# Kernel optimization log

Hardware: AMD Instinct MI355X
Metric: run time of the kernel (lower is better)

Reference implementation:

```python
import jax, jax.numpy as jnp
import numpy as np
import math

B, S, D, H = 2, 2048, 1024, 16
HD = D // H


def _rms_norm(x, scale):
    # norm over (seq, d_model) jointly per batch element, as in the source
    b, s, d = x.shape
    ff_rms = jnp.sqrt(jnp.sum(x * x, axis=(1, 2))) * (s * d) ** -0.5  # (B,)
    return scale[None, :s, :] * (x / ff_rms[:, None, None])


def _rope(x):
    # faithful to _generate_rope_matrix: theta = 10000^(-2*(i-1)/D) (note i-1)
    b, s, d = x.shape
    i = jnp.arange(d // 2, dtype=jnp.float32)
    theta = 10000.0 ** (-2.0 * (i - 1.0) / d)            # (D/2,)
    ang = jnp.arange(s, dtype=jnp.float32)[:, None] * theta[None, :]  # (S, D/2)
    cos, sin = jnp.cos(ang), jnp.sin(ang)
    xp = x.reshape(b, s, d // 2, 2)
    xe, xo = xp[..., 0], xp[..., 1]
    # out = x @ R[pos]; R block [[cos,-sin],[sin,cos]] per pair
    oe = xe * cos + xo * sin
    oo = -xe * sin + xo * cos
    return jnp.stack([oe, oo], axis=-1).reshape(b, s, d)


def _alibi_mask(s, h):
    r = jnp.arange(s)
    dist = r[:, None] - r[None, :]                        # row j - col i
    base = jnp.where(dist < 0, -jnp.inf, -dist.astype(jnp.float32))  # (S,S)
    ratio = 2.0 ** (-8.0 / h)
    slopes = ratio ** jnp.arange(1, h + 1, dtype=jnp.float32)        # (H,)
    return base[None, :, :] * slopes[:, None, None]       # (H,S,S)


def setup_inputs() -> dict:
    key = jax.random.key(0)
    ks = jax.random.split(key, 9)
    p = lambda k, shp: jax.random.normal(k, shp, jnp.float32) * 0.02
    return {
        "x": jax.random.normal(ks[0], (B, S, D), jnp.float32),
        "Wq": p(ks[1], (D, D)), "Wk": p(ks[2], (D, D)),
        "Wv": p(ks[3], (D, D)), "Wo": p(ks[4], (D, D)),
        "scale1": jnp.ones((S, D), jnp.float32),
        "scale2": jnp.ones((S, D), jnp.float32),
        "W1": p(ks[5], (D, D)), "b1": jnp.zeros((D,), jnp.float32),
        "Wg": p(ks[6], (D, D)), "bg": jnp.zeros((D,), jnp.float32),
        "Wl": p(ks[7], (D, D)), "bl": jnp.zeros((D,), jnp.float32),
        "beta": jnp.ones((1,), jnp.float32),
    }


def reference(x, Wq, Wk, Wv, Wo, scale1, scale2, W1, b1, Wg, bg, Wl, bl, beta):
    b, s, d = x.shape
    # --- attention sublayer ---
    h = _rms_norm(x, scale1)
    q = _rope(h @ Wq)
    k = _rope(h @ Wk)
    v = _rope(h @ Wv)
    qh = q.reshape(b, s, H, HD).transpose(0, 2, 1, 3)  # (B,H,S,HD)
    kh = k.reshape(b, s, H, HD).transpose(0, 2, 1, 3)
    vh = v.reshape(b, s, H, HD).transpose(0, 2, 1, 3)
    mask = _alibi_mask(s, H)                           # (H,S,S)
    scores = jnp.einsum("bhqd,bhkd->bhqk", qh, kh) * (1.0 / math.sqrt(HD))
    probs = jax.nn.softmax(scores + mask[None], axis=-1)
    o = jnp.einsum("bhqk,bhkd->bhqd", probs, vh)
    o = o.transpose(0, 2, 1, 3).reshape(b, s, d)
    x_res_1 = x + o @ Wo
    # --- FFN sublayer: Linear -> SwiGLU ---
    h2 = _rms_norm(x_res_1, scale2) @ W1 + b1
    g = h2 @ Wg + bg
    swish_gate = g * jax.nn.sigmoid(beta * g)
    ffn = swish_gate * (h2 @ Wl + bl)
    return x_res_1 + ffn
```

## Files before the change

### kernel.cpp

```cpp
#include <hip/hip_runtime.h>
#include <hip/hip_bf16.h>

typedef __attribute__((ext_vector_type(8))) short bf16x8;
typedef __attribute__((ext_vector_type(4))) float f32x4;
typedef __attribute__((ext_vector_type(4))) int int4v;

#define DEV static __device__ __forceinline__

DEV float b2f(unsigned short u) { union { unsigned int i; float f; } c; c.i = ((unsigned int)u) << 16; return c.f; }
DEV unsigned short f2b(float f) {
  __hip_bfloat16 h = __float2bfloat16(f);
  unsigned short u; __builtin_memcpy(&u, &h, 2); return u;
}

DEV void gload16(const void* g, void* l) {
  __builtin_amdgcn_global_load_lds(
      (const __attribute__((address_space(1))) unsigned int*)(g),
      (__attribute__((address_space(3))) unsigned int*)(l), 16, 0, 0);
}

__global__ __launch_bounds__(256) void k_transpose_w7(const float* __restrict__ Wq,
                                                      const float* __restrict__ Wk,
                                                      const float* __restrict__ Wv,
                                                      const float* __restrict__ Wo,
                                                      const float* __restrict__ W1,
                                                      const float* __restrict__ Wg,
                                                      const float* __restrict__ Wl,
                                                      unsigned short* __restrict__ WT) {
  __shared__ float tile[32][33];
  const float* W;
  switch (blockIdx.z) {
    case 0: W = Wq; break; case 1: W = Wk; break; case 2: W = Wv; break;
    case 3: W = Wo; break; case 4: W = W1; break; case 5: W = Wg; break;
    default: W = Wl; break;
  }
  unsigned short* dst = WT + (size_t)blockIdx.z * 1048576;
  const int tx = threadIdx.x & 31, ty = threadIdx.x >> 5;
  const int c0 = blockIdx.x * 32, r0 = blockIdx.y * 32;
#pragma unroll
  for (int i = 0; i < 4; ++i)
    tile[ty + i * 8][tx] = W[(size_t)(r0 + ty + i * 8) * 1024 + c0 + tx];
  __syncthreads();
#pragma unroll
  for (int i = 0; i < 4; ++i)
    dst[(size_t)(c0 + ty + i * 8) * 1024 + r0 + tx] = f2b(tile[tx][ty + i * 8]);
}

__global__ __launch_bounds__(256) void k_reduce_sq(const float* __restrict__ x,
                                                   float* __restrict__ sums) {
  const int b = blockIdx.y;
  const float4* xb = (const float4*)(x + (size_t)b * 2097152);
  float s = 0.f;
  for (int i = blockIdx.x * 256 + threadIdx.x; i < 524288; i += 256 * gridDim.x) {
    float4 v = xb[i];
    s += v.x * v.x + v.y * v.y + v.z * v.z + v.w * v.w;
  }
  __shared__ float red[256];
  red[threadIdx.x] = s;
  __syncthreads();
  for (int st = 128; st > 0; st >>= 1) {
    if (threadIdx.x < st) red[threadIdx.x] += red[threadIdx.x + st];
    __syncthreads();
  }
  if (threadIdx.x == 0) atomicAdd(&sums[b], red[0]);
}

__global__ __launch_bounds__(256) void k_rmsnorm(const float* __restrict__ x,
                                                 const float* __restrict__ scale,
                                                 const float* __restrict__ sums,
                                                 unsigned short* __restrict__ out) {
  const int idx = blockIdx.x * 256 + threadIdx.x;
  const int e = idx * 4;
  const int m = e >> 10, d = e & 1023;
  const int b = m >> 11, s = m & 2047;
  const float inv = rsqrtf(sums[b] * (1.0f / 2097152.0f));
  float4 xv = *(const float4*)(x + (size_t)e);
  float4 sv = *(const float4*)(scale + (size_t)s * 1024 + d);
  ushort4 o;
  o.x = f2b(xv.x * sv.x * inv); o.y = f2b(xv.y * sv.y * inv);
  o.z = f2b(xv.z * sv.z * inv); o.w = f2b(xv.w * sv.w * inv);
  *(ushort4*)(out + e) = o;
}

template <int EPI, int NREP>
__global__ __launch_bounds__(256) void k_gemm(const unsigned short* __restrict__ A,
                                              const unsigned short* __restrict__ Bt,
                                              void* __restrict__ Cout,
                                              const float* __restrict__ aux,
                                              const float* __restrict__ aux2,
                                              const float* __restrict__ x1p,
                                              const float* __restrict__ betap,
                                              const int N,
                                              float* __restrict__ ss) {
  constexpr int BN = NREP * 32;
  __shared__ short As[2][128 * 64];
  __shared__ short Bs[2][BN * 64];
  const int tid = threadIdx.x;
  const int w = tid >> 6, l = tid & 63;
  const int brow = blockIdx.y * 128;
  const int bcol = blockIdx.x * (EPI == 4 ? 64 : BN);
  const int wr = (w >> 1) * 64;
  const int wc = (EPI == 4) ? (w & 1) * 32 : (w & 1) * (NREP * 16);
  const int lr = l >> 3, lg = l & 7;
  f32x4 acc[4][NREP] = {};
  const short* Ag = (const short*)A;
  const short* Bg = (const short*)Bt;

  auto STAGE = [&](int buf, int k0) {
#pragma unroll
    for (int p = 0; p < 4; ++p) {
      const int row = p * 32 + w * 8 + lr;
      gload16(Ag + (size_t)(brow + row) * 1024 + k0 + lg * 8,
              (char*)&As[buf][0] + (size_t)(p * 32 + w * 8) * 128);
    }
#pragma unroll
    for (int p = 0; p < NREP; ++p) {
      const int row = p * 32 + w * 8 + lr;
      size_t goff;
      if (EPI == 4 && p >= 2)
        goff = (size_t)1048576 + (size_t)(bcol + row - 64) * 1024;
      else
        goff = (size_t)(bcol + row) * 1024;
      gload16(Bg + goff + k0 + lg * 8,
              (char*)&Bs[buf][0] + (size_t)(p * 32 + w * 8) * 128);
    }
  };

  STAGE(0, 0);
  __syncthreads();
  int cur = 0;
  for (int t = 0; t < 16; ++t) {
    if (t < 15) STAGE(cur ^ 1, (t + 1) * 64);
#pragma unroll
    for (int kk = 0; kk < 2; ++kk) {
      const int g0 = kk * 4 + (l >> 4);
      bf16x8 af[4], bfr[NREP];
#pragma unroll
      for (int m = 0; m < 4; ++m)
        af[m] = *(const bf16x8*)(&As[cur][0] + (wr + m * 16 + (l & 15)) * 64 + g0 * 8);
#pragma unroll
      for (int n = 0; n < NREP; ++n) {
        int bsrow;
        if (EPI == 4) bsrow = (n < 2) ? (wc + n * 16 + (l & 15)) : (64 + wc + (n - 2) * 16 + (l & 15));
        else bsrow = wc + n * 16 + (l & 15);
        bfr[n] = *(const bf16x8*)(&Bs[cur][0] + bsrow * 64 + g0 * 8);
      }
      __builtin_amdgcn_s_setprio(1);
#pragma unroll
      for (int m = 0; m < 4; ++m)
#pragma unroll
        for (int n = 0; n < NREP; ++n)
          acc[m][n] = __builtin_amdgcn_mfma_f32_16x16x32_bf16(af[m], bfr[n], acc[m][n], 0, 0, 0);
      __builtin_amdgcn_s_setprio(0);
    }
    __syncthreads();
    cur ^= 1;
  }
  const int rr = (l >> 4) * 4, cc = l & 15;
  if (EPI == 5) {
    const bool dorope = (bcol < 2048);
    if (dorope) {
      float th[NREP];
#pragma unroll
      for (int n = 0; n < NREP; ++n)
        th[n] = exp2f(-((float)(((bcol + wc + n * 16 + cc) & 1023) >> 1) - 1.0f) * 0.0259525627f);
#pragma unroll
      for (int m = 0; m < 4; ++m)
#pragma unroll
        for (int n = 0; n < NREP; ++n) {
          const int col = bcol + wc + n * 16 + cc;
#pragma unroll
          for (int j = 0; j < 4; ++j) {
            const int row = brow + wr + m * 16 + rr + j;
            const float vo = acc[m][n][j];
            const float vp = __shfl_xor(vo, 1);
            float sn, cs;
            __sincosf((float)(row & 2047) * th[n], &sn, &cs);
            const float r = (cc & 1) ? (cs * vo - sn * vp) : (cs * vo + sn * vp);
            ((unsigned short*)Cout)[(size_t)row * N + col] = f2b(r);
          }
        }
    } else {
#pragma unroll
      for (int m = 0; m < 4; ++m)
#pragma unroll
        for (int n = 0; n < NREP; ++n) {
          const int col = bcol + wc + n * 16 + cc;
#pragma unroll
          for (int j = 0; j < 4; ++j) {
            const int row = brow + wr + m * 16 + rr + j;
            ((unsigned short*)Cout)[(size_t)row * N + col] = f2b(acc[m][n][j]);
          }
        }
    }
    return;
  }
  if (EPI == 4) {
    const float bt = betap[0];
#pragma unroll
    for (int m = 0; m < 4; ++m)
#pragma unroll
      for (int nn = 0; nn < 2; ++nn) {
        const int col = bcol + wc + nn * 16 + cc;
#pragma unroll
        for (int j = 0; j < 4; ++j) {
          const int row = brow + wr + m * 16 + rr + j;
          const float gv = acc[m][nn][j] + aux[col];
          const float lv = acc[m][nn + 2][j] + aux2[col];
          const float sw = gv / (1.f + __expf(-bt * gv));
          ((float*)Cout)[(size_t)row * 1024 + col] = x1p[(size_t)row * 1024 + col] + sw * lv;
        }
      }
    return;
  }
  float sq = 0.f;
#pragma unroll
  for (int m = 0; m < 4; ++m)
#pragma unroll
    for (int n = 0; n < NREP; ++n) {
      const int col = bcol + wc + n * 16 + cc;
#pragma unroll
      for (int j = 0; j < 4; ++j) {
        const int row = brow + wr + m * 16 + rr + j;
        float v = acc[m][n][j];
        if (EPI == 1) {
          const float v2 = aux[(size_t)row * N + col] + v;
          ((float*)Cout)[(size_t)row * N + col] = v2;
          sq += v2 * v2;
        } else {
          ((unsigned short*)Cout)[(size_t)row * N + col] = f2b(v + aux[col]);
        }
      }
    }
  if (EPI == 1) {
#pragma unroll
    for (int off = 1; off < 64; off <<= 1) sq += __shfl_xor(sq, off);
    if (l == 0) atomicAdd(&ss[brow >> 11], sq);
  }
}

__global__ __launch_bounds__(256) void k_transpose_v(const unsigned short* __restrict__ qkv,
                                                     unsigned short* __restrict__ vt) {
  __shared__ unsigned short tile[32][33];
  const int tx = threadIdx.x & 31, ty = threadIdx.x >> 5;
  const int bh = blockIdx.z;
  const int b = bh >> 4, h = bh & 15;
  const int d0 = blockIdx.x * 32, s0 = blockIdx.y * 32;
#pragma unroll
  for (int i = 0; i < 4; ++i)
    tile[ty + i * 8][tx] = qkv[(size_t)(b * 2048 + s0 + ty + i * 8) * 3072 + 2048 + h * 64 + d0 + tx];
  __syncthreads();
  const float sv = (float)(s0 + tx);
  const int par = ty & 1;
#pragma unroll
  for (int i = 0; i < 4; ++i) {
    const int dsec = h * 64 + d0 + ty + i * 8;
    const float th = exp2f(-((float)(dsec >> 1) - 1.0f) * 0.0259525627f);
    float sn, cs;
    __sincosf(sv * th, &sn, &cs);
    const float vo = b2f(tile[tx][ty + i * 8]);
    const float vp = b2f(tile[tx][(ty ^ 1) + i * 8]);
    const float r = par ? (cs * vo - sn * vp) : (cs * vo + sn * vp);
    vt[((size_t)bh * 64 + d0 + ty + i * 8) * 2048 + s0 + tx] = f2b(r);
  }
}

__global__ __launch_bounds__(256) void k_attn(const unsigned short* __restrict__ qkv,
                                              const unsigned short* __restrict__ vt,
                                              unsigned short* __restrict__ o) {
  __shared__ short Ks[2][4096];
  __shared__ short Vs[2][4096];
  __shared__ short Ps[8][1280];
  const int id = blockIdx.x;
  const int xcd = id & 7, q = id >> 3;
  const int p = q & 15, g = (q >> 4) * 8 + xcd;
  const int h = g & 15, b = g >> 4;
  const int qtA = p, qtB = 31 - p;
  const int nA = qtA + 1, nB = qtB + 1;
  const int tid = threadIdx.x, w = tid >> 6, l = tid & 63;
  const int cc = l & 15, hi = l >> 4;
  const int qwA = qtA * 64 + w * 16, qwB = qtB * 64 + w * 16;
  const short* qg = (const short*)qkv;
  bf16x8 aqA0, aqA1, aqB0, aqB1;
  {
    const short* baseA = qg + (size_t)(b * 2048 + qwA + cc) * 3072 + h * 64 + hi * 8;
    aqA0 = *(const bf16x8*)baseA;
    aqA1 = *(const bf16x8*)(baseA + 32);
    const short* baseB = qg + (size_t)(b * 2048 + qwB + cc) * 3072 + h * 64 + hi * 8;
    aqB0 = *(const bf16x8*)baseB;
    aqB1 = *(const bf16x8*)(baseB + 32);
  }
  const float slope2 = exp2f(-0.5f * (float)(h + 1)) * 1.44269504f;
  const float C1 = 0.125f * 1.44269504f;
  const float step = slope2 * 64.f;
  bf16x8 onesf;
#pragma unroll
  for (int z = 0; z < 8; ++z) onesf[z] = (short)0x3F80;
  f32x4 oaccA[4] = {}, oaccB[4] = {};
  f32x4 rsA = {}, rsB = {};
  float baseA4[4], baseB4[4];
#pragma unroll
  for (int n = 0; n < 4; ++n) {
    baseA4[n] = slope2 * (float)(n * 16 + cc - qwA - hi * 4);
    baseB4[n] = slope2 * (float)(n * 16 + cc - qwB - hi * 4);
  }
  short* PwA = &Ps[w][0];
  short* PwB = &Ps[w + 4][0];
  const int c0 = tid, c1 = tid + 256;
  const int r0 = c0 >> 3, g0c = c0 & 7;
  const int r1 = c1 >> 3, g1c = c1 & 7;
  const int s0 = r0 * 64 + ((g0c ^ (r0 & 7)) * 8);
  const int s1 = r1 * 64 + ((g1c ^ (r1 & 7)) * 8);
  const short* kbase = qg + (size_t)(b * 2048) * 3072 + 1024 + h * 64;
  const short* vbase = (const short*)vt + (size_t)(b * 16 + h) * 64 * 2048;
  *(int4v*)(&Ks[0][s0]) = *(const int4v*)(kbase + (size_t)r0 * 3072 + g0c * 8);
  *(int4v*)(&Ks[0][s1]) = *(const int4v*)(kbase + (size_t)r1 * 3072 + g1c * 8);
  *(int4v*)(&Vs[0][s0]) = *(const int4v*)(vbase + (size_t)r0 * 2048 + g0c * 8);
  *(int4v*)(&Vs[0][s1]) = *(const int4v*)(vbase + (size_t)r1 * 2048 + g1c * 8);
  __syncthreads();

  auto sm_pv = [&](f32x4 (&sacc)[4], f32x4 (&oacc)[4], f32x4& rs, float (&base)[4],
                   short* Pw, const int qw, const bool domask, const int kv0,
                   const short* Vsc) {
#pragma unroll
    for (int n = 0; n < 4; ++n) {
#pragma unroll
      for (int j = 0; j < 4; ++j) {
        float v = fmaf(sacc[n][j], C1, base[n] - slope2 * (float)j);
        if (domask) {
          const int kvg = kv0 + n * 16 + cc;
          const int qrow = qw + hi * 4 + j;
          if (kvg > qrow) v = -1e30f;
        }
        Pw[(hi * 4 + j) * 80 + n * 16 + cc] = (short)f2b(exp2f(v));
      }
      base[n] += step;
    }
    __builtin_amdgcn_s_setprio(1);
#pragma unroll
    for (int kk2 = 0; kk2 < 2; ++kk2) {
      bf16x8 pf = *(const bf16x8*)(Pw + cc * 80 + kk2 * 32 + hi * 8);
      rs = __builtin_amdgcn_mfma_f32_16x16x32_bf16(pf, onesf, rs, 0, 0, 0);
#pragma unroll
      for (int n = 0; n < 4; ++n) {
        const int dr = n * 16 + cc;
        bf16x8 vf = *(const bf16x8*)(Vsc + dr * 64 + (((kk2 * 4 + hi) ^ (dr & 7)) * 8));
        oacc[n] = __builtin_amdgcn_mfma_f32_16x16x32_bf16(pf, vf, oacc[n], 0, 0, 0);
      }
    }
    __builtin_amdgcn_s_setprio(0);
  };

  int cur = 0;
  for (int t = 0; t < nB; ++t) {
    int4v kr0, kr1, vr0, vr1;
    const bool havenext = (t + 1 < nB);
    if (havenext) {
      const size_t k0n = (size_t)(t + 1) * 64;
      kr0 = *(const int4v*)(kbase + (k0n + r0) * 3072 + g0c * 8);
      kr1 = *(const int4v*)(kbase + (k0n + r1) * 3072 + g1c * 8);
      vr0 = *(const int4v*)(vbase + (size_t)r0 * 2048 + k0n + g0c * 8);
      vr1 = *(const int4v*)(vbase + (size_t)r1 * 2048 + k0n + g1c * 8);
    }
    const int kv0 = t * 64;
    const short* Ksc = &Ks[cur][0];
    const short* Vsc = &Vs[cur][0];
    const bool doA = (t < nA);
    f32x4 sB[4] = {}, sA[4] = {};
    __builtin_amdgcn_s_setprio(1);
#pragma unroll
    for (int kk = 0; kk < 2; ++kk) {
      const int g0r = kk * 4 + hi;
      const bf16x8 aqk = kk ? aqB1 : aqB0;
#pragma unroll
      for (int n = 0; n < 4; ++n) {
        const int col = n * 16 + cc;
        bf16x8 bk = *(const bf16x8*)(Ksc + col * 64 + ((g0r ^ (col & 7)) * 8));
        sB[n] = __builtin_amdgcn_mfma_f32_16x16x32_bf16(aqk, bk, sB[n], 0, 0, 0);
      }
    }
    if (doA) {
#pragma unroll
      for (int kk = 0; kk < 2; ++kk) {
        const int g0r = kk * 4 + hi;
        const bf16x8 aqk = kk ? aqA1 : aqA0;
#pragma unroll
        for (int n = 0; n < 4; ++n) {
          const int col = n * 16 + cc;
          bf16x8 bk = *(const bf16x8*)(Ksc + col * 64 + ((g0r ^ (col & 7)) * 8));
          sA[n] = __builtin_amdgcn_mfma_f32_16x16x32_bf16(aqk, bk, sA[n], 0, 0, 0);
        }
      }
    }
    __builtin_amdgcn_s_setprio(0);
    sm_pv(sB, oaccB, rsB, baseB4, PwB, qwB, t == nB - 1, kv0, Vsc);
    if (doA) sm_pv(sA, oaccA, rsA, baseA4, PwA, qwA, t == nA - 1, kv0, Vsc);
    if (havenext) {
      const int nxt = cur ^ 1;
      *(int4v*)(&Ks[nxt][s0]) = kr0;
      *(int4v*)(&Ks[nxt][s1]) = kr1;
      *(int4v*)(&Vs[nxt][s0]) = vr0;
      *(int4v*)(&Vs[nxt][s1]) = vr1;
    }
    __syncthreads();
    cur ^= 1;
  }
  {
    const int rr = hi * 4;
#pragma unroll
    for (int n = 0; n < 4; ++n)
#pragma unroll
      for (int j = 0; j < 4; ++j) {
        const int row = qwA + rr + j;
        o[(size_t)(b * 2048 + row) * 1024 + h * 64 + n * 16 + cc] = f2b(oaccA[n][j] / rsA[j]);
      }
#pragma unroll
    for (int n = 0; n < 4; ++n)
#pragma unroll
      for (int j = 0; j < 4; ++j) {
        const int row = qwB + rr + j;
        o[(size_t)(b * 2048 + row) * 1024 + h * 64 + n * 16 + cc] = f2b(oaccB[n][j] / rsB[j]);
      }
  }
}

extern "C" void kernel_launch(void* const* d_in, const int* in_sizes, int n_in,
                              void* d_out, int out_size, void* d_ws, size_t ws_size,
                              hipStream_t stream) {
  (void)in_sizes; (void)n_in; (void)out_size; (void)ws_size;
  const float* x      = (const float*)d_in[0];
  const float* Wq     = (const float*)d_in[1];
  const float* Wk     = (const float*)d_in[2];
  const float* Wv     = (const float*)d_in[3];
  const float* Wo     = (const float*)d_in[4];
  const float* scale1 = (const float*)d_in[5];
  const float* scale2 = (const float*)d_in[6];
  const float* W1     = (const float*)d_in[7];
  const float* b1     = (const float*)d_in[8];
  const float* Wg     = (const float*)d_in[9];
  const float* bg     = (const float*)d_in[10];
  const float* Wl     = (const float*)d_in[11];
  const float* bl     = (const float*)d_in[12];
  const float* beta   = (const float*)d_in[13];
  float* out = (float*)d_out;

  char* ws = (char*)d_ws;
  float* sums         = (float*)ws;
  unsigned short* WT  = (unsigned short*)(ws + 16384);
  unsigned short* h   = (unsigned short*)(ws + 16384 + 14680064);
  unsigned short* qkv = (unsigned short*)((char*)h + 8388608);
  unsigned short* vt  = (unsigned short*)((char*)qkv + 25165824);
  float* x1           = (float*)((char*)vt + 8388608);
  unsigned short* ob  = h;
  unsigned short* t1  = qkv;

  hipMemsetAsync(sums, 0, 256, stream);

  k_transpose_w7<<<dim3(32, 32, 7), 256, 0, stream>>>(Wq, Wk, Wv, Wo, W1, Wg, Wl, WT);
  k_reduce_sq<<<dim3(256, 2), 256, 0, stream>>>(x, sums);
  k_rmsnorm<<<4096, 256, 0, stream>>>(x, scale1, sums, h);
  k_gemm<5, 4><<<dim3(24, 32), 256, 0, stream>>>(h, WT, (void*)qkv, nullptr, nullptr, nullptr, nullptr, 3072, nullptr);
  k_transpose_v<<<dim3(2, 64, 32), 256, 0, stream>>>(qkv, vt);
  k_attn<<<512, 256, 0, stream>>>(qkv, vt, ob);
  k_gemm<1, 2><<<dim3(16, 32), 256, 0, stream>>>(ob, WT + 3145728, (void*)x1, x, nullptr, nullptr, nullptr, 1024, sums + 2);

  k_rmsnorm<<<4096, 256, 0, stream>>>(x1, scale2, sums + 2, h);
  k_gemm<2, 2><<<dim3(16, 32), 256, 0, stream>>>(h, WT + 4194304, (void*)t1, b1, nullptr, nullptr, nullptr, 1024, nullptr);
  k_gemm<4, 4><<<dim3(16, 32), 256, 0, stream>>>(t1, WT + 5242880, (void*)out, bg, bl, x1, beta, 1024, nullptr);
}
```

Before: 344.1 us.

## Split paired causal query tiles into one tile per attention block

The attention kernel used to give each block two query tiles (p and 31-p) so every block had the same causal work, and both tiles shared each K/V tile loaded into LDS. Now each block handles a single query tile, the grid doubles to 1024 blocks, and tile order is rotated by head index. This lowers register and LDS use per block, which should allow more blocks per CU. In exchange, K/V tiles are loaded twice as often overall and blocks have uneven causal work.

After: 342.2 us. Within noise of the previous version (-0.6%).

```diff
diff --git a/kernel.cpp b/kernel.cpp
--- a/kernel.cpp
+++ b/kernel.cpp
@@ -270,25 +270,21 @@
                                               unsigned short* __restrict__ o) {
   __shared__ short Ks[2][4096];
   __shared__ short Vs[2][4096];
-  __shared__ short Ps[8][1280];
+  __shared__ short Ps[4][1280];
   const int id = blockIdx.x;
-  const int xcd = id & 7, q = id >> 3;
-  const int p = q & 15, g = (q >> 4) * 8 + xcd;
+  const int g = id >> 5;
+  const int qt = ((id & 31) + g) & 31;
   const int h = g & 15, b = g >> 4;
-  const int qtA = p, qtB = 31 - p;
-  const int nA = qtA + 1, nB = qtB + 1;
+  const int nt = qt + 1;
   const int tid = threadIdx.x, w = tid >> 6, l = tid & 63;
   const int cc = l & 15, hi = l >> 4;
-  const int qwA = qtA * 64 + w * 16, qwB = qtB * 64 + w * 16;
+  const int qw = qt * 64 + w * 16;
   const short* qg = (const short*)qkv;
-  bf16x8 aqA0, aqA1, aqB0, aqB1;
+  bf16x8 aq0, aq1;
   {
-    const short* baseA = qg + (size_t)(b * 2048 + qwA + cc) * 3072 + h * 64 + hi * 8;
-    aqA0 = *(const bf16x8*)baseA;
-    aqA1 = *(const bf16x8*)(baseA + 32);
-    const short* baseB = qg + (size_t)(b * 2048 + qwB + cc) * 3072 + h * 64 + hi * 8;
-    aqB0 = *(const bf16x8*)baseB;
-    aqB1 = *(const bf16x8*)(baseB + 32);
+    const short* base = qg + (size_t)(b * 2048 + qw + cc) * 3072 + h * 64 + hi * 8;
+    aq0 = *(const bf16x8*)base;
+    aq1 = *(const bf16x8*)(base + 32);
   }
   const float slope2 = exp2f(-0.5f * (float)(h + 1)) * 1.44269504f;
   const float C1 = 0.125f * 1.44269504f;
@@ -296,16 +292,13 @@
   bf16x8 onesf;
 #pragma unroll
   for (int z = 0; z < 8; ++z) onesf[z] = (short)0x3F80;
-  f32x4 oaccA[4] = {}, oaccB[4] = {};
-  f32x4 rsA = {}, rsB = {};
-  float baseA4[4], baseB4[4];
-#pragma unroll
-  for (int n = 0; n < 4; ++n) {
-    baseA4[n] = slope2 * (float)(n * 16 + cc - qwA - hi * 4);
-    baseB4[n] = slope2 * (float)(n * 16 + cc - qwB - hi * 4);
-  }
-  short* PwA = &Ps[w][0];
-  short* PwB = &Ps[w + 4][0];
+  f32x4 oacc[4] = {};
+  f32x4 rs = {};
+  float base4[4];
+#pragma unroll
+  for (int n = 0; n < 4; ++n)
+    base4[n] = slope2 * (float)(n * 16 + cc - qw - hi * 4);
+  short* Pw = &Ps[w][0];
   const int c0 = tid, c1 = tid + 256;
   const int r0 = c0 >> 3, g0c = c0 & 7;
   const int r1 = c1 >> 3, g1c = c1 & 7;
@@ -319,14 +312,40 @@
   *(int4v*)(&Vs[0][s1]) = *(const int4v*)(vbase + (size_t)r1 * 2048 + g1c * 8);
   __syncthreads();
 
-  auto sm_pv = [&](f32x4 (&sacc)[4], f32x4 (&oacc)[4], f32x4& rs, float (&base)[4],
-                   short* Pw, const int qw, const bool domask, const int kv0,
-                   const short* Vsc) {
+  int cur = 0;
+  for (int t = 0; t < nt; ++t) {
+    int4v kr0, kr1, vr0, vr1;
+    const bool havenext = (t + 1 < nt);
+    if (havenext) {
+      const size_t k0n = (size_t)(t + 1) * 64;
+      kr0 = *(const int4v*)(kbase + (k0n + r0) * 3072 + g0c * 8);
+      kr1 = *(const int4v*)(kbase + (k0n + r1) * 3072 + g1c * 8);
+      vr0 = *(const int4v*)(vbase + (size_t)r0 * 2048 + k0n + g0c * 8);
+      vr1 = *(const int4v*)(vbase + (size_t)r1 * 2048 + k0n + g1c * 8);
+    }
+    const int kv0 = t * 64;
+    const short* Ksc = &Ks[cur][0];
+    const short* Vsc = &Vs[cur][0];
+    f32x4 sacc[4] = {};
+    __builtin_amdgcn_s_setprio(1);
+#pragma unroll
+    for (int kk = 0; kk < 2; ++kk) {
+      const int g0r = kk * 4 + hi;
+      const bf16x8 aqk = kk ? aq1 : aq0;
+#pragma unroll
+      for (int n = 0; n < 4; ++n) {
+        const int col = n * 16 + cc;
+        bf16x8 bk = *(const bf16x8*)(Ksc + col * 64 + ((g0r ^ (col & 7)) * 8));
+        sacc[n] = __builtin_amdgcn_mfma_f32_16x16x32_bf16(aqk, bk, sacc[n], 0, 0, 0);
+      }
+    }
+    __builtin_amdgcn_s_setprio(0);
+    const bool domask = (t == nt - 1);
 #pragma unroll
     for (int n = 0; n < 4; ++n) {
 #pragma unroll
       for (int j = 0; j < 4; ++j) {
-        float v = fmaf(sacc[n][j], C1, base[n] - slope2 * (float)j);
+        float v = fmaf(sacc[n][j], C1, base4[n] - slope2 * (float)j);
         if (domask) {
           const int kvg = kv0 + n * 16 + cc;
           const int qrow = qw + hi * 4 + j;
@@ -334,7 +353,7 @@
         }
         Pw[(hi * 4 + j) * 80 + n * 16 + cc] = (short)f2b(exp2f(v));
       }
-      base[n] += step;
+      base4[n] += step;
     }
     __builtin_amdgcn_s_setprio(1);
 #pragma unroll
@@ -349,52 +368,6 @@
       }
     }
     __builtin_amdgcn_s_setprio(0);
-  };
-
-  int cur = 0;
-  for (int t = 0; t < nB; ++t) {
-    int4v kr0, kr1, vr0, vr1;
-    const bool havenext = (t + 1 < nB);
-    if (havenext) {
-      const size_t k0n = (size_t)(t + 1) * 64;
-      kr0 = *(const int4v*)(kbase + (k0n + r0) * 3072 + g0c * 8);
-      kr1 = *(const int4v*)(kbase + (k0n + r1) * 3072 + g1c * 8);
-      vr0 = *(const int4v*)(vbase + (size_t)r0 * 2048 + k0n + g0c * 8);
-      vr1 = *(const int4v*)(vbase + (size_t)r1 * 2048 + k0n + g1c * 8);
-    }
-    const int kv0 = t * 64;
-    const short* Ksc = &Ks[cur][0];
-    const short* Vsc = &Vs[cur][0];
-    const bool doA = (t < nA);
-    f32x4 sB[4] = {}, sA[4] = {};
-    __builtin_amdgcn_s_setprio(1);
-#pragma unroll
-    for (int kk = 0; kk < 2; ++kk) {
-      const int g0r = kk * 4 + hi;
-      const bf16x8 aqk = kk ? aqB1 : aqB0;
-#pragma unroll
-      for (int n = 0; n < 4; ++n) {
-        const int col = n * 16 + cc;
-        bf16x8 bk = *(const bf16x8*)(Ksc + col * 64 + ((g0r ^ (col & 7)) * 8));
-        sB[n] = __builtin_amdgcn_mfma_f32_16x16x32_bf16(aqk, bk, sB[n], 0, 0, 0);
-      }
-    }
-    if (doA) {
-#pragma unroll
-      for (int kk = 0; kk < 2; ++kk) {
-        const int g0r = kk * 4 + hi;
-        const bf16x8 aqk = kk ? aqA1 : aqA0;
-#pragma unroll
-        for (int n = 0; n < 4; ++n) {
-          const int col = n * 16 + cc;
-          bf16x8 bk = *(const bf16x8*)(Ksc + col * 64 + ((g0r ^ (col & 7)) * 8));
-          sA[n] = __builtin_amdgcn_mfma_f32_16x16x32_bf16(aqk, bk, sA[n], 0, 0, 0);
-        }
-      }
-    }
-    __builtin_amdgcn_s_setprio(0);
-    sm_pv(sB, oaccB, rsB, baseB4, PwB, qwB, t == nB - 1, kv0, Vsc);
-    if (doA) sm_pv(sA, oaccA, rsA, baseA4, PwA, qwA, t == nA - 1, kv0, Vsc);
     if (havenext) {
       const int nxt = cur ^ 1;
       *(int4v*)(&Ks[nxt][s0]) = kr0;
@@ -411,15 +384,8 @@
     for (int n = 0; n < 4; ++n)
 #pragma unroll
       for (int j = 0; j < 4; ++j) {
-        const int row = qwA + rr + j;
-        o[(size_t)(b * 2048 + row) * 1024 + h * 64 + n * 16 + cc] = f2b(oaccA[n][j] / rsA[j]);
-      }
-#pragma unroll
-    for (int n = 0; n < 4; ++n)
-#pragma unroll
-      for (int j = 0; j < 4; ++j) {
-        const int row = qwB + rr + j;
-        o[(size_t)(b * 2048 + row) * 1024 + h * 64 + n * 16 + cc] = f2b(oaccB[n][j] / rsB[j]);
+        const int row = qw + rr + j;
+        o[(size_t)(b * 2048 + row) * 1024 + h * 64 + n * 16 + cc] = f2b(oacc[n][j] / rs[j]);
       }
   }
 }
@@ -461,7 +427,7 @@
   k_rmsnorm<<<4096, 256, 0, stream>>>(x, scale1, sums, h);
   k_gemm<5, 4><<<dim3(24, 32), 256, 0, stream>>>(h, WT, (void*)qkv, nullptr, nullptr, nullptr, nullptr, 3072, nullptr);
   k_transpose_v<<<dim3(2, 64, 32), 256, 0, stream>>>(qkv, vt);
-  k_attn<<<512, 256, 0, stream>>>(qkv, vt, ob);
+  k_attn<<<1024, 256, 0, stream>>>(qkv, vt, ob);
   k_gemm<1, 2><<<dim3(16, 32), 256, 0, stream>>>(ob, WT + 3145728, (void*)x1, x, nullptr, nullptr, nullptr, 1024, sums + 2);
 
   k_rmsnorm<<<4096, 256, 0, stream>>>(x1, scale2, sums + 2, h);
```
